# Kernel optimization log

Hardware: AMD Instinct MI355X
Metric: run time of the kernel (lower is better)

Reference implementation:

```python
import jax, jax.numpy as jnp
import numpy as np

V, NLAB, NLAYERS, DI, DM, DS, DD, K = 32000, 9, 2, 768, 1536, 16, 96, 4
B, S = 2, 2048
EPS = 1e-6


def setup_inputs() -> dict:
    key = jax.random.key(0)
    ks = jax.random.split(key, 12)
    n = lambda k, shape, s=0.02: jax.random.normal(k, shape, jnp.float32) * s
    return {
        "input_ids": jax.random.randint(ks[0], (B, S), 0, V, dtype=jnp.int32),
        "attention_mask": jnp.ones((B, S), jnp.int32),
        "emb": n(ks[1], (V, DI)),
        "norm_w": jnp.ones((NLAYERS, DI), jnp.float32),
        "in_proj_w": n(ks[2], (NLAYERS, 2 * DM, DI)),
        "conv_w": n(ks[3], (NLAYERS, DM, K), 0.1),
        "conv_b": jnp.zeros((NLAYERS, DM), jnp.float32),
        "sB_w": n(ks[4], (NLAYERS, DS, DM)),
        "sC_w": n(ks[5], (NLAYERS, DS, DM)),
        "sD1_w": n(ks[6], (NLAYERS, DD, DM)),
        "sD2_w": n(ks[7], (NLAYERS, DM, DD)),
        "A": jnp.tile(jnp.arange(1, DS + 1, dtype=jnp.float32), (NLAYERS, DM, 1)),
        "Dp": jnp.ones((NLAYERS, DM), jnp.float32),
        "out_w": n(ks[8], (NLAYERS, DI, DM)),
        "cls_w": n(ks[9], (NLAB, DI)),
        "cls_b": jnp.zeros((NLAB,), jnp.float32),
    }


def _rmsnorm(x, w):
    return x * jax.lax.rsqrt(jnp.mean(x * x, axis=-1, keepdims=True) + EPS) * w


def _mamba_block(x, norm_w, Wi, cw, cb, WB, WC, W1, W2, A, Dp, Wo):
    # x: (b, l, d_input)
    h = _rmsnorm(x, norm_w)
    a, gate = jnp.split(h @ Wi.T, 2, axis=-1)  # each (b, l, DM)
    # causal depthwise conv1d, kernel K, left-pad K-1 (== Conv1d(pad=K-1)[..., :l])
    L = a.shape[1]
    ap = jnp.pad(a, ((0, 0), (K - 1, 0), (0, 0)))
    conv = cb + sum(ap[:, i:i + L, :] * cw[:, i] for i in range(K))
    a = jax.nn.silu(conv)
    # selective SSM
    Bm = a @ WB.T                                   # (b, l, DS)
    Cm = a @ WC.T                                   # (b, l, DS)
    delta = jax.nn.softplus(Dp + (a @ W1.T) @ W2.T)  # (b, l, DM)
    A_bar = jnp.exp(delta[..., None] * (-A))         # (b, l, DM, DS)
    X_bar = (delta * a)[..., None] * Bm[:, :, None, :]  # (b, l, DM, DS)

    def comb(c1, c2):
        a1, x1 = c1
        a2, x2 = c2
        return a1 * a2, a2 * x1 + x2

    _, hid = jax.lax.associative_scan(comb, (A_bar, X_bar), axis=1)
    y = jnp.einsum('blds,bls->bld', hid, Cm) + Dp * a
    y = y * jax.nn.silu(gate)
    return y @ Wo.T


def _forward(input_ids, attention_mask, emb, norm_w, in_proj_w, conv_w, conv_b,
             sB_w, sC_w, sD1_w, sD2_w, A, Dp, out_w, cls_w, cls_b):
    x = emb[input_ids] * attention_mask[..., None].astype(emb.dtype)
    for i in range(NLAYERS):  # residual Mamba layers
        x = _mamba_block(x, norm_w[i], in_proj_w[i], conv_w[i], conv_b[i],
                         sB_w[i], sC_w[i], sD1_w[i], sD2_w[i], A[i], Dp[i], out_w[i]) + x
    # dropout is identity at inference
    return x @ cls_w.T + cls_b  # logits (b, l, num_labels)


def reference(input_ids, attention_mask, emb, norm_w, in_proj_w, conv_w, conv_b,
              sB_w, sC_w, sD1_w, sD2_w, A, Dp, out_w, cls_w, cls_b):
    return _forward(input_ids, attention_mask, emb, norm_w, in_proj_w, conv_w, conv_b,
                    sB_w, sC_w, sD1_w, sD2_w, A, Dp, out_w, cls_w, cls_b)
```

## Files before the change

### kernel.cpp

```cpp
#include <hip/hip_runtime.h>
#include <hip/hip_bf16.h>
#include <math.h>

#define NLAB 9
#define NL   2
#define DI   768
#define DM   1536
#define DS   16
#define KC   4
#define DD   96
#define BB   2
#define SS   2048
#define TT   (BB*SS)
#define EPSF 1e-6f

#define NCH  64
#define CL   (SS/NCH)

#define NW   128
#define KS   8
#define KSL  (DM/KS)

typedef __attribute__((ext_vector_type(4))) float f32x4;
typedef __attribute__((ext_vector_type(8))) short bf16x8;
typedef __attribute__((ext_vector_type(4))) unsigned short us4;

__device__ __forceinline__ float siluf(float x) { return x / (1.f + __expf(-x)); }
__device__ __forceinline__ float softplusf(float x) { return x > 15.f ? x : log1pf(__expf(x)); }

__device__ __forceinline__ unsigned short f2bf(float f) {
    unsigned u = __float_as_uint(f);
    return (unsigned short)((u + 0x7fffu + ((u >> 16) & 1u)) >> 16);
}

__global__ void f32_to_bf16(const float* __restrict__ src,
                            unsigned short* __restrict__ dst, int n)
{
    int i = (blockIdx.x * 256 + threadIdx.x) * 8;
    if (i >= n) return;
    float4 a = *(const float4*)(src + i);
    float4 b = *(const float4*)(src + i + 4);
    union { unsigned short s[8]; uint4 v; } o;
    o.s[0] = f2bf(a.x); o.s[1] = f2bf(a.y); o.s[2] = f2bf(a.z); o.s[3] = f2bf(a.w);
    o.s[4] = f2bf(b.x); o.s[5] = f2bf(b.y); o.s[6] = f2bf(b.z); o.s[7] = f2bf(b.w);
    *(uint4*)(dst + i) = o.v;
}

__global__ void embed_kernel(const int* __restrict__ ids, const int* __restrict__ mask,
                             const float* __restrict__ emb, float* __restrict__ x)
{
    int t = blockIdx.x;
    int i = threadIdx.x;
    float m = (float)mask[t];
    int id = ids[t];
    float4 v = ((const float4*)(emb + (size_t)id * DI))[i];
    v.x *= m; v.y *= m; v.z *= m; v.w *= m;
    ((float4*)(x + (size_t)t * DI))[i] = v;
}

__global__ void rmsnorm_kernel(const float* __restrict__ x, const float* __restrict__ w,
                               unsigned short* __restrict__ h)
{
    __shared__ float red[4];
    int t = blockIdx.x;
    const float* xr = x + (size_t)t * DI;
    float ss = 0.f;
    for (int i = threadIdx.x; i < DI; i += 256) { float v = xr[i]; ss += v * v; }
    #pragma unroll
    for (int m = 1; m < 64; m <<= 1) ss += __shfl_xor(ss, m, 64);
    if ((threadIdx.x & 63) == 0) red[threadIdx.x >> 6] = ss;
    __syncthreads();
    float scale = rsqrtf((red[0] + red[1] + red[2] + red[3]) * (1.f / DI) + EPSF);
    for (int i = threadIdx.x; i < DI; i += 256)
        h[(size_t)t * DI + i] = f2bf(xr[i] * scale * w[i]);
}

__global__ __launch_bounds__(256) void gemm_bf16(
    const unsigned short* __restrict__ A, const unsigned short* __restrict__ B,
    const float* __restrict__ Rres, const float* __restrict__ bias,
    float* __restrict__ C, int M, int N, int K,
    int lda, int ldb, int ldc, int act, int cstride)
{
    __shared__ unsigned short As[128 * 32];
    __shared__ unsigned short Bs[128 * 32];
    const int tid = threadIdx.x;
    const int wave = tid >> 6, lane = tid & 63;
    const int bm = blockIdx.y * 128, bn = blockIdx.x * 128;
    const int wm = (wave >> 1) * 64, wn = (wave & 1) * 64;
    const int lr = lane & 15, kh = lane >> 4;

    f32x4 acc[4][4] = {};

    const unsigned short* Arow = A + (size_t)bm * lda;
    const unsigned short* Brow = B + (size_t)bn * ldb;

    for (int kt = 0; kt < K; kt += 32) {
        #pragma unroll
        for (int it = 0; it < 2; ++it) {
            int rbase = it * 64 + wave * 16;
            int row = rbase + (lane >> 2);
            int c8 = (lane & 3) * 8;
            __builtin_amdgcn_global_load_lds(
                (const __attribute__((address_space(1))) unsigned int*)(Arow + (size_t)row * lda + kt + c8),
                (__attribute__((address_space(3))) unsigned int*)(As + rbase * 32),
                16, 0, 0);
            __builtin_amdgcn_global_load_lds(
                (const __attribute__((address_space(1))) unsigned int*)(Brow + (size_t)row * ldb + kt + c8),
                (__attribute__((address_space(3))) unsigned int*)(Bs + rbase * 32),
                16, 0, 0);
        }
        __syncthreads();

        bf16x8 af[4], bfr[4];
        #pragma unroll
        for (int i = 0; i < 4; ++i)
            af[i] = *(const bf16x8*)&As[(wm + i * 16 + lr) * 32 + kh * 8];
        #pragma unroll
        for (int j = 0; j < 4; ++j)
            bfr[j] = *(const bf16x8*)&Bs[(wn + j * 16 + lr) * 32 + kh * 8];
        #pragma unroll
        for (int i = 0; i < 4; ++i)
            #pragma unroll
            for (int j = 0; j < 4; ++j)
                acc[i][j] = __builtin_amdgcn_mfma_f32_16x16x32_bf16(af[i], bfr[j], acc[i][j], 0, 0, 0);
        __syncthreads();
    }

    #pragma unroll
    for (int i = 0; i < 4; ++i) {
        #pragma unroll
        for (int j = 0; j < 4; ++j) {
            #pragma unroll
            for (int r = 0; r < 4; ++r) {
                int row = bm + wm + i * 16 + kh * 4 + r;
                int col = bn + wn + j * 16 + lr;
                float v = acc[i][j][r];
                if (bias) v += bias[col];
                if (act == 1) v = softplusf(v);
                if (Rres) v += Rres[(size_t)row * ldc + col];
                C[((size_t)row * ldc + col) * cstride] = v;
            }
        }
    }
}

__global__ __launch_bounds__(256) void gemm_skinny_bf16(
    const unsigned short* __restrict__ A, const unsigned short* __restrict__ B,
    float* __restrict__ Part)
{
    __shared__ unsigned short As[128 * 32];
    __shared__ unsigned short Bs[128 * 32];
    const int tid = threadIdx.x;
    const int wave = tid >> 6, lane = tid & 63;
    const int bm = blockIdx.x * 128;
    const int ks = blockIdx.y;
    const int k0 = ks * KSL;
    const int wm = (wave >> 1) * 64, wn = (wave & 1) * 64;
    const int lr = lane & 15, kh = lane >> 4;

    f32x4 acc[4][4] = {};

    const unsigned short* Arow = A + (size_t)bm * DM;
    const unsigned short* Brow = B;

    for (int kt = 0; kt < KSL; kt += 32) {
        #pragma unroll
        for (int it = 0; it < 2; ++it) {
            int rbase = it * 64 + wave * 16;
            int row = rbase + (lane >> 2);
            int c8 = (lane & 3) * 8;
            __builtin_amdgcn_global_load_lds(
                (const __attribute__((address_space(1))) unsigned int*)(Arow + (size_t)row * DM + k0 + kt + c8),
                (__attribute__((address_space(3))) unsigned int*)(As + rbase * 32),
                16, 0, 0);
            __builtin_amdgcn_global_load_lds(
                (const __attribute__((address_space(1))) unsigned int*)(Brow + (size_t)row * DM + k0 + kt + c8),
                (__attribute__((address_space(3))) unsigned int*)(Bs + rbase * 32),
                16, 0, 0);
        }
        __syncthreads();

        bf16x8 af[4], bfr[4];
        #pragma unroll
        for (int i = 0; i < 4; ++i)
            af[i] = *(const bf16x8*)&As[(wm + i * 16 + lr) * 32 + kh * 8];
        #pragma unroll
        for (int j = 0; j < 4; ++j)
            bfr[j] = *(const bf16x8*)&Bs[(wn + j * 16 + lr) * 32 + kh * 8];
        #pragma unroll
        for (int i = 0; i < 4; ++i)
            #pragma unroll
            for (int j = 0; j < 4; ++j)
                acc[i][j] = __builtin_amdgcn_mfma_f32_16x16x32_bf16(af[i], bfr[j], acc[i][j], 0, 0, 0);
        __syncthreads();
    }

    float* out = Part + (size_t)ks * TT * NW;
    #pragma unroll
    for (int i = 0; i < 4; ++i) {
        #pragma unroll
        for (int j = 0; j < 4; ++j) {
            #pragma unroll
            for (int r = 0; r < 4; ++r) {
                int row = bm + wm + i * 16 + kh * 4 + r;
                int col = wn + j * 16 + lr;
                out[(size_t)row * NW + col] = acc[i][j][r];
            }
        }
    }
}

__global__ void skinny_reduce(const float* __restrict__ Part,
                              float* __restrict__ BCD, unsigned short* __restrict__ dd16)
{
    int idx = blockIdx.x * 256 + threadIdx.x;
    float s = 0.f;
    #pragma unroll
    for (int ks = 0; ks < KS; ++ks)
        s += Part[(size_t)ks * TT * NW + idx];
    BCD[idx] = s;
    int col = idx & (NW - 1);
    if (col >= 32)
        dd16[(size_t)(idx >> 7) * DD + (col - 32)] = f2bf(s);
}

__global__ void conv_silu_kernel(const float* __restrict__ proj, const float* __restrict__ cw,
                                 const float* __restrict__ cb, float2* __restrict__ dav,
                                 unsigned short* __restrict__ aconv16)
{
    int t = blockIdx.x;
    int d = blockIdx.y * 256 + threadIdx.x;
    int p = t & (SS - 1);
    float acc = cb[d];
    #pragma unroll
    for (int j = 0; j < KC; ++j) {
        int pp = p - (KC - 1) + j;
        if (pp >= 0)
            acc += cw[d * KC + j] * proj[(size_t)(t - (KC - 1) + j) * (2 * DM) + d];
    }
    float v = siluf(acc);
    dav[(size_t)t * DM + d].y = v;
    aconv16[(size_t)t * DM + d] = f2bf(v);
}

__global__ void concat_w_kernel(const float* __restrict__ WB, const float* __restrict__ WC,
                                const float* __restrict__ W1, unsigned short* __restrict__ Wcat16)
{
    int l = blockIdx.y;
    int row = blockIdx.x;
    const float* src;
    if (row < 16)      src = WB + (size_t)l * DS * DM + (size_t)row * DM;
    else if (row < 32) src = WC + (size_t)l * DS * DM + (size_t)(row - 16) * DM;
    else               src = W1 + (size_t)l * DD * DM + (size_t)(row - 32) * DM;
    unsigned short* dst = Wcat16 + ((size_t)l * NW + row) * DM;
    for (int i = threadIdx.x; i < DM / 4; i += 256) {
        float4 v = ((const float4*)src)[i];
        us4 u = { f2bf(v.x), f2bf(v.y), f2bf(v.z), f2bf(v.w) };
        *(us4*)(dst + i * 4) = u;
    }
}

__global__ __launch_bounds__(256) void scan_pass1(
    const float2* __restrict__ dav,
    const float* __restrict__ BCD, const float* __restrict__ Amat,
    float2* __restrict__ PQ)
{
    __shared__ float4 sB4[CL][DS / 4];
    int b = blockIdx.z, c = blockIdx.y;
    int d = blockIdx.x * 256 + threadIdx.x;
    size_t rowbase = (size_t)b * SS + (size_t)c * CL;

    for (int i = threadIdx.x; i < CL * DS; i += 256)
        ((float*)sB4)[i] = BCD[(rowbase + (i >> 4)) * NW + (i & 15)];
    __syncthreads();

    float negA[DS], hid[DS];
    #pragma unroll
    for (int s = 0; s < DS; ++s) {
        negA[s] = -Amat[(size_t)d * DS + s];
        hid[s] = 0.f;
    }
    float cum = 0.f;

    const float2* pv = dav + rowbase * DM + d;
    for (int t = 0; t < CL; ++t) {
        float2 da = pv[(size_t)t * DM];
        float dt = da.x, av = da.y;
        cum += dt;
        float xv = dt * av;
        #pragma unroll
        for (int j = 0; j < DS / 4; ++j) {
            float4 bv = sB4[t][j];
            hid[4*j+0] = __expf(dt * negA[4*j+0]) * hid[4*j+0] + xv * bv.x;
            hid[4*j+1] = __expf(dt * negA[4*j+1]) * hid[4*j+1] + xv * bv.y;
            hid[4*j+2] = __expf(dt * negA[4*j+2]) * hid[4*j+2] + xv * bv.z;
            hid[4*j+3] = __expf(dt * negA[4*j+3]) * hid[4*j+3] + xv * bv.w;
        }
    }
    float2* out = PQ + ((size_t)(b * NCH + c) * DM + d) * DS;
    #pragma unroll
    for (int s = 0; s < DS; ++s)
        out[s] = make_float2(__expf(cum * negA[s]), hid[s]);
}

__global__ void scan_carry(float2* __restrict__ PQ)
{
    int idx = blockIdx.x * 256 + threadIdx.x;
    int b = idx / (DM * DS);
    int r = idx - b * (DM * DS);
    float carry = 0.f;
    for (int c = 0; c < NCH; ++c) {
        size_t o = (size_t)(b * NCH + c) * (DM * DS) + r;
        float2 pq = PQ[o];
        PQ[o].x = carry;
        carry = pq.x * carry + pq.y;
    }
}

__global__ __launch_bounds__(256) void scan_pass2(
    const float2* __restrict__ dav,
    const float* __restrict__ BCD,
    const float* __restrict__ proj, const float* __restrict__ Amat,
    const float* __restrict__ Dp, const float2* __restrict__ PQ,
    unsigned short* __restrict__ y)
{
    __shared__ float4 sB4[CL][DS / 4];
    __shared__ float4 sC4[CL][DS / 4];
    int b = blockIdx.z, c = blockIdx.y;
    int d = blockIdx.x * 256 + threadIdx.x;
    size_t rowbase = (size_t)b * SS + (size_t)c * CL;

    for (int i = threadIdx.x; i < CL * DS; i += 256) {
        size_t row = rowbase + (i >> 4);
        ((float*)sB4)[i] = BCD[row * NW + (i & 15)];
        ((float*)sC4)[i] = BCD[row * NW + 16 + (i & 15)];
    }
    __syncthreads();

    float negA[DS], hid[DS];
    const float2* pin = PQ + ((size_t)(b * NCH + c) * DM + d) * DS;
    #pragma unroll
    for (int s = 0; s < DS; ++s) {
        negA[s] = -Amat[(size_t)d * DS + s];
        hid[s] = pin[s].x;
    }
    float Dpd = Dp[d];

    const float2* pv = dav + rowbase * DM + d;
    const float* gp = proj + rowbase * (2 * DM) + DM + d;
    unsigned short* yp = y + rowbase * DM + d;

    for (int t = 0; t < CL; ++t) {
        float2 da = pv[(size_t)t * DM];
        float dt = da.x, av = da.y;
        float g  = gp[(size_t)t * (2 * DM)];
        float xv = dt * av;
        float acc0 = 0.f, acc1 = 0.f, acc2 = 0.f, acc3 = 0.f;
        #pragma unroll
        for (int j = 0; j < DS / 4; ++j) {
            float4 bv = sB4[t][j];
            float4 cv = sC4[t][j];
            hid[4*j+0] = __expf(dt * negA[4*j+0]) * hid[4*j+0] + xv * bv.x;
            hid[4*j+1] = __expf(dt * negA[4*j+1]) * hid[4*j+1] + xv * bv.y;
            hid[4*j+2] = __expf(dt * negA[4*j+2]) * hid[4*j+2] + xv * bv.z;
            hid[4*j+3] = __expf(dt * negA[4*j+3]) * hid[4*j+3] + xv * bv.w;
            acc0 += hid[4*j+0] * cv.x;
            acc1 += hid[4*j+1] * cv.y;
            acc2 += hid[4*j+2] * cv.z;
            acc3 += hid[4*j+3] * cv.w;
        }
        float contrib = (acc0 + acc1) + (acc2 + acc3);
        yp[(size_t)t * DM] = f2bf((contrib + Dpd * av) * siluf(g));
    }
}

__global__ void cls_kernel(const float* __restrict__ x, const float* __restrict__ W,
                           const float* __restrict__ bias, float* __restrict__ out)
{
    int t = blockIdx.x;
    int lane = threadIdx.x;
    const float* xr = x + (size_t)t * DI;
    float acc[NLAB];
    #pragma unroll
    for (int n = 0; n < NLAB; ++n) acc[n] = 0.f;
    for (int i = lane; i < DI; i += 64) {
        float xv = xr[i];
        #pragma unroll
        for (int n = 0; n < NLAB; ++n) acc[n] += xv * W[(size_t)n * DI + i];
    }
    #pragma unroll
    for (int n = 0; n < NLAB; ++n)
        #pragma unroll
        for (int m = 1; m < 64; m <<= 1) acc[n] += __shfl_xor(acc[n], m, 64);
    if (lane < NLAB) out[(size_t)t * NLAB + lane] = acc[lane] + bias[lane];
}

extern "C" void kernel_launch(void* const* d_in, const int* in_sizes, int n_in,
                              void* d_out, int out_size, void* d_ws, size_t ws_size,
                              hipStream_t stream)
{
    const int*   ids    = (const int*)d_in[0];
    const int*   mask   = (const int*)d_in[1];
    const float* emb    = (const float*)d_in[2];
    const float* norm_w = (const float*)d_in[3];
    const float* Wi     = (const float*)d_in[4];
    const float* conv_w = (const float*)d_in[5];
    const float* conv_b = (const float*)d_in[6];
    const float* sB_w   = (const float*)d_in[7];
    const float* sC_w   = (const float*)d_in[8];
    const float* sD1_w  = (const float*)d_in[9];
    const float* sD2_w  = (const float*)d_in[10];
    const float* Amat   = (const float*)d_in[11];
    const float* Dp     = (const float*)d_in[12];
    const float* out_w  = (const float*)d_in[13];
    const float* cls_w  = (const float*)d_in[14];
    const float* cls_b  = (const float*)d_in[15];
    float* logits = (float*)d_out;

    float* ws = (float*)d_ws;
    size_t off = 0;
    float* x     = ws + off; off += (size_t)TT * DI;
    float* proj  = ws + off; off += (size_t)TT * 2 * DM;
    float2* dav  = (float2*)(ws + off); off += (size_t)TT * DM * 2;
    float* BCD   = ws + off; off += (size_t)TT * NW;
    size_t scratch_sz = (size_t)BB * NCH * DM * DS * 2;
    size_t part_sz = (size_t)KS * TT * NW;
    if (part_sz > scratch_sz) scratch_sz = part_sz;
    float* Part  = ws + off;
    float2* PQ   = (float2*)(ws + off); off += scratch_sz;
    unsigned short* y16     = (unsigned short*)(ws + off); off += (size_t)TT * DM / 2;
    unsigned short* aconv16 = (unsigned short*)(ws + off); off += (size_t)TT * DM / 2;
    unsigned short* Wi16    = (unsigned short*)(ws + off); off += (size_t)NL * 2 * DM * DI / 2;
    unsigned short* Wo16    = (unsigned short*)(ws + off); off += (size_t)NL * DI * DM / 2;
    unsigned short* W216    = (unsigned short*)(ws + off); off += (size_t)NL * DM * DD / 2;
    unsigned short* dd16    = (unsigned short*)(ws + off); off += (size_t)TT * DD / 2;
    unsigned short* Wcat16  = (unsigned short*)(ws + off); off += (size_t)NL * NW * DM / 2;
    if (ws_size < off * sizeof(float)) return;

    unsigned short* h16 = (unsigned short*)dav;

    embed_kernel<<<TT, DI / 4, 0, stream>>>(ids, mask, emb, x);
    concat_w_kernel<<<dim3(NW, NL), 256, 0, stream>>>(sB_w, sC_w, sD1_w, Wcat16);

    f32_to_bf16<<<(NL * 2 * DM * DI / 8 + 255) / 256, 256, 0, stream>>>(Wi, Wi16, NL * 2 * DM * DI);
    f32_to_bf16<<<(NL * DI * DM / 8 + 255) / 256, 256, 0, stream>>>(out_w, Wo16, NL * DI * DM);
    f32_to_bf16<<<(NL * DM * DD / 8 + 255) / 256, 256, 0, stream>>>(sD2_w, W216, NL * DM * DD);

    for (int l = 0; l < NL; ++l) {
        const float* cw_l  = conv_w + (size_t)l * DM * KC;
        const float* cb_l  = conv_b + (size_t)l * DM;
        const float* A_l   = Amat  + (size_t)l * DM * DS;
        const float* Dp_l  = Dp    + (size_t)l * DM;
        const float* nw_l  = norm_w + (size_t)l * DI;
        const unsigned short* Wi16_l  = Wi16  + (size_t)l * 2 * DM * DI;
        const unsigned short* Wo16_l  = Wo16  + (size_t)l * DI * DM;
        const unsigned short* W216_l  = W216  + (size_t)l * DM * DD;
        const unsigned short* Wcat16_l = Wcat16 + (size_t)l * NW * DM;

        rmsnorm_kernel<<<TT, 256, 0, stream>>>(x, nw_l, h16);

        gemm_bf16<<<dim3(2 * DM / 128, TT / 128), 256, 0, stream>>>(
            h16, Wi16_l, nullptr, nullptr, proj, TT, 2 * DM, DI, DI, DI, 2 * DM, 0, 1);

        conv_silu_kernel<<<dim3(TT, DM / 256), 256, 0, stream>>>(proj, cw_l, cb_l, dav, aconv16);

        gemm_skinny_bf16<<<dim3(TT / 128, KS), 256, 0, stream>>>(aconv16, Wcat16_l, Part);
        skinny_reduce<<<TT * NW / 256, 256, 0, stream>>>(Part, BCD, dd16);

        gemm_bf16<<<dim3(DM / 128, TT / 128), 256, 0, stream>>>(
            dd16, W216_l, nullptr, Dp_l, (float*)dav, TT, DM, DD, DD, DD, DM, 1, 2);

        scan_pass1<<<dim3(DM / 256, NCH, BB), 256, 0, stream>>>(dav, BCD, A_l, PQ);
        scan_carry<<<BB * DM * DS / 256, 256, 0, stream>>>(PQ);
        scan_pass2<<<dim3(DM / 256, NCH, BB), 256, 0, stream>>>(
            dav, BCD, proj, A_l, Dp_l, PQ, y16);

        gemm_bf16<<<dim3(DI / 128, TT / 128), 256, 0, stream>>>(
            y16, Wo16_l, x, nullptr, x, TT, DI, DM, DM, DM, DI, 0, 1);
    }

    cls_kernel<<<TT, 64, 0, stream>>>(x, cls_w, cls_b, logits);
}
```

Measured before the change: 786.2 us.

## Double-buffer LDS tiles in GEMMs and split interleaved delta/activation buffer

```diff
diff --git a/kernel.cpp b/kernel.cpp
--- a/kernel.cpp
+++ b/kernel.cpp
@@ -75,14 +75,45 @@
         h[(size_t)t * DI + i] = f2bf(xr[i] * scale * w[i]);
 }
 
+#define STAGE_TILE(AS, BS, KT) do {                                                           \
+    _Pragma("unroll")                                                                         \
+    for (int it = 0; it < 2; ++it) {                                                          \
+        int rbase = it * 64 + wave * 16;                                                      \
+        int row = rbase + (lane >> 2);                                                        \
+        int c8 = (lane & 3) * 8;                                                              \
+        __builtin_amdgcn_global_load_lds(                                                     \
+            (const __attribute__((address_space(1))) unsigned int*)(Arow + (size_t)row * lda + (KT) + c8), \
+            (__attribute__((address_space(3))) unsigned int*)((AS) + rbase * 32), 16, 0, 0);  \
+        __builtin_amdgcn_global_load_lds(                                                     \
+            (const __attribute__((address_space(1))) unsigned int*)(Brow + (size_t)row * ldb + (KT) + c8), \
+            (__attribute__((address_space(3))) unsigned int*)((BS) + rbase * 32), 16, 0, 0);  \
+    } } while (0)
+
+#define COMPUTE_TILE(AS, BS) do {                                                             \
+    bf16x8 af[4], bfr[4];                                                                     \
+    _Pragma("unroll")                                                                         \
+    for (int i = 0; i < 4; ++i)                                                               \
+        af[i] = *(const bf16x8*)&(AS)[(wm + i * 16 + lr) * 32 + kh * 8];                      \
+    _Pragma("unroll")                                                                         \
+    for (int j = 0; j < 4; ++j)                                                               \
+        bfr[j] = *(const bf16x8*)&(BS)[(wn + j * 16 + lr) * 32 + kh * 8];                     \
+    _Pragma("unroll")                                                                         \
+    for (int i = 0; i < 4; ++i)                                                               \
+        _Pragma("unroll")                                                                     \
+        for (int j = 0; j < 4; ++j)                                                           \
+            acc[i][j] = __builtin_amdgcn_mfma_f32_16x16x32_bf16(af[i], bfr[j], acc[i][j], 0, 0, 0); \
+    } while (0)
+
 __global__ __launch_bounds__(256) void gemm_bf16(
     const unsigned short* __restrict__ A, const unsigned short* __restrict__ B,
     const float* __restrict__ Rres, const float* __restrict__ bias,
     float* __restrict__ C, int M, int N, int K,
     int lda, int ldb, int ldc, int act, int cstride)
 {
-    __shared__ unsigned short As[128 * 32];
-    __shared__ unsigned short Bs[128 * 32];
+    __shared__ unsigned short As0[128 * 32];
+    __shared__ unsigned short Bs0[128 * 32];
+    __shared__ unsigned short As1[128 * 32];
+    __shared__ unsigned short Bs1[128 * 32];
     const int tid = threadIdx.x;
     const int wave = tid >> 6, lane = tid & 63;
     const int bm = blockIdx.y * 128, bn = blockIdx.x * 128;
@@ -94,36 +125,21 @@
     const unsigned short* Arow = A + (size_t)bm * lda;
     const unsigned short* Brow = B + (size_t)bn * ldb;
 
-    for (int kt = 0; kt < K; kt += 32) {
-        #pragma unroll
-        for (int it = 0; it < 2; ++it) {
-            int rbase = it * 64 + wave * 16;
-            int row = rbase + (lane >> 2);
-            int c8 = (lane & 3) * 8;
-            __builtin_amdgcn_global_load_lds(
-                (const __attribute__((address_space(1))) unsigned int*)(Arow + (size_t)row * lda + kt + c8),
-                (__attribute__((address_space(3))) unsigned int*)(As + rbase * 32),
-                16, 0, 0);
-            __builtin_amdgcn_global_load_lds(
-                (const __attribute__((address_space(1))) unsigned int*)(Brow + (size_t)row * ldb + kt + c8),
-                (__attribute__((address_space(3))) unsigned int*)(Bs + rbase * 32),
-                16, 0, 0);
-        }
+    STAGE_TILE(As0, Bs0, 0);
+    __syncthreads();
+
+    int kt = 0;
+    while (true) {
+        if (kt + 32 < K) STAGE_TILE(As1, Bs1, kt + 32);
+        COMPUTE_TILE(As0, Bs0);
         __syncthreads();
-
-        bf16x8 af[4], bfr[4];
-        #pragma unroll
-        for (int i = 0; i < 4; ++i)
-            af[i] = *(const bf16x8*)&As[(wm + i * 16 + lr) * 32 + kh * 8];
-        #pragma unroll
-        for (int j = 0; j < 4; ++j)
-            bfr[j] = *(const bf16x8*)&Bs[(wn + j * 16 + lr) * 32 + kh * 8];
-        #pragma unroll
-        for (int i = 0; i < 4; ++i)
-            #pragma unroll
-            for (int j = 0; j < 4; ++j)
-                acc[i][j] = __builtin_amdgcn_mfma_f32_16x16x32_bf16(af[i], bfr[j], acc[i][j], 0, 0, 0);
+        kt += 32;
+        if (kt >= K) break;
+        if (kt + 32 < K) STAGE_TILE(As0, Bs0, kt + 32);
+        COMPUTE_TILE(As1, Bs1);
         __syncthreads();
+        kt += 32;
+        if (kt >= K) break;
     }
 
     #pragma unroll
@@ -148,8 +164,10 @@
     const unsigned short* __restrict__ A, const unsigned short* __restrict__ B,
     float* __restrict__ Part)
 {
-    __shared__ unsigned short As[128 * 32];
-    __shared__ unsigned short Bs[128 * 32];
+    __shared__ unsigned short As0[128 * 32];
+    __shared__ unsigned short Bs0[128 * 32];
+    __shared__ unsigned short As1[128 * 32];
+    __shared__ unsigned short Bs1[128 * 32];
     const int tid = threadIdx.x;
     const int wave = tid >> 6, lane = tid & 63;
     const int bm = blockIdx.x * 128;
@@ -157,42 +175,28 @@
     const int k0 = ks * KSL;
     const int wm = (wave >> 1) * 64, wn = (wave & 1) * 64;
     const int lr = lane & 15, kh = lane >> 4;
+    const int lda = DM, ldb = DM;
 
     f32x4 acc[4][4] = {};
 
     const unsigned short* Arow = A + (size_t)bm * DM;
     const unsigned short* Brow = B;
 
-    for (int kt = 0; kt < KSL; kt += 32) {
-        #pragma unroll
-        for (int it = 0; it < 2; ++it) {
-            int rbase = it * 64 + wave * 16;
-            int row = rbase + (lane >> 2);
-            int c8 = (lane & 3) * 8;
-            __builtin_amdgcn_global_load_lds(
-                (const __attribute__((address_space(1))) unsigned int*)(Arow + (size_t)row * DM + k0 + kt + c8),
-                (__attribute__((address_space(3))) unsigned int*)(As + rbase * 32),
-                16, 0, 0);
-            __builtin_amdgcn_global_load_lds(
-                (const __attribute__((address_space(1))) unsigned int*)(Brow + (size_t)row * DM + k0 + kt + c8),
-                (__attribute__((address_space(3))) unsigned int*)(Bs + rbase * 32),
-                16, 0, 0);
-        }
+    STAGE_TILE(As0, Bs0, k0);
+    __syncthreads();
+
+    int kt = 0;
+    while (true) {
+        if (kt + 32 < KSL) STAGE_TILE(As1, Bs1, k0 + kt + 32);
+        COMPUTE_TILE(As0, Bs0);
         __syncthreads();
-
-        bf16x8 af[4], bfr[4];
-        #pragma unroll
-        for (int i = 0; i < 4; ++i)
-            af[i] = *(const bf16x8*)&As[(wm + i * 16 + lr) * 32 + kh * 8];
-        #pragma unroll
-        for (int j = 0; j < 4; ++j)
-            bfr[j] = *(const bf16x8*)&Bs[(wn + j * 16 + lr) * 32 + kh * 8];
-        #pragma unroll
-        for (int i = 0; i < 4; ++i)
-            #pragma unroll
-            for (int j = 0; j < 4; ++j)
-                acc[i][j] = __builtin_amdgcn_mfma_f32_16x16x32_bf16(af[i], bfr[j], acc[i][j], 0, 0, 0);
+        kt += 32;
+        if (kt >= KSL) break;
+        if (kt + 32 < KSL) STAGE_TILE(As0, Bs0, k0 + kt + 32);
+        COMPUTE_TILE(As1, Bs1);
         __syncthreads();
+        kt += 32;
+        if (kt >= KSL) break;
     }
 
     float* out = Part + (size_t)ks * TT * NW;
@@ -225,7 +229,7 @@
 }
 
 __global__ void conv_silu_kernel(const float* __restrict__ proj, const float* __restrict__ cw,
-                                 const float* __restrict__ cb, float2* __restrict__ dav,
+                                 const float* __restrict__ cb, float* __restrict__ av,
                                  unsigned short* __restrict__ aconv16)
 {
     int t = blockIdx.x;
@@ -239,7 +243,7 @@
             acc += cw[d * KC + j] * proj[(size_t)(t - (KC - 1) + j) * (2 * DM) + d];
     }
     float v = siluf(acc);
-    dav[(size_t)t * DM + d].y = v;
+    av[(size_t)t * DM + d] = v;
     aconv16[(size_t)t * DM + d] = f2bf(v);
 }
 
@@ -261,7 +265,7 @@
 }
 
 __global__ __launch_bounds__(256) void scan_pass1(
-    const float2* __restrict__ dav,
+    const float* __restrict__ dtv, const float* __restrict__ av,
     const float* __restrict__ BCD, const float* __restrict__ Amat,
     float2* __restrict__ PQ)
 {
@@ -282,12 +286,13 @@
     }
     float cum = 0.f;
 
-    const float2* pv = dav + rowbase * DM + d;
+    const float* pd = dtv + rowbase * DM + d;
+    const float* pa = av  + rowbase * DM + d;
     for (int t = 0; t < CL; ++t) {
-        float2 da = pv[(size_t)t * DM];
-        float dt = da.x, av = da.y;
+        float dt = pd[(size_t)t * DM];
+        float avv = pa[(size_t)t * DM];
         cum += dt;
-        float xv = dt * av;
+        float xv = dt * avv;
         #pragma unroll
         for (int j = 0; j < DS / 4; ++j) {
             float4 bv = sB4[t][j];
@@ -318,7 +323,7 @@
 }
 
 __global__ __launch_bounds__(256) void scan_pass2(
-    const float2* __restrict__ dav,
+    const float* __restrict__ dtv, const float* __restrict__ av,
     const float* __restrict__ BCD,
     const float* __restrict__ proj, const float* __restrict__ Amat,
     const float* __restrict__ Dp, const float2* __restrict__ PQ,
@@ -346,15 +351,16 @@
     }
     float Dpd = Dp[d];
 
-    const float2* pv = dav + rowbase * DM + d;
+    const float* pd = dtv + rowbase * DM + d;
+    const float* pa = av  + rowbase * DM + d;
     const float* gp = proj + rowbase * (2 * DM) + DM + d;
     unsigned short* yp = y + rowbase * DM + d;
 
     for (int t = 0; t < CL; ++t) {
-        float2 da = pv[(size_t)t * DM];
-        float dt = da.x, av = da.y;
+        float dt = pd[(size_t)t * DM];
+        float avv = pa[(size_t)t * DM];
         float g  = gp[(size_t)t * (2 * DM)];
-        float xv = dt * av;
+        float xv = dt * avv;
         float acc0 = 0.f, acc1 = 0.f, acc2 = 0.f, acc3 = 0.f;
         #pragma unroll
         for (int j = 0; j < DS / 4; ++j) {
@@ -370,7 +376,7 @@
             acc3 += hid[4*j+3] * cv.w;
         }
         float contrib = (acc0 + acc1) + (acc2 + acc3);
-        yp[(size_t)t * DM] = f2bf((contrib + Dpd * av) * siluf(g));
+        yp[(size_t)t * DM] = f2bf((contrib + Dpd * avv) * siluf(g));
     }
 }
 
@@ -421,7 +427,8 @@
     size_t off = 0;
     float* x     = ws + off; off += (size_t)TT * DI;
     float* proj  = ws + off; off += (size_t)TT * 2 * DM;
-    float2* dav  = (float2*)(ws + off); off += (size_t)TT * DM * 2;
+    float* dtv   = ws + off; off += (size_t)TT * DM;
+    float* av    = ws + off; off += (size_t)TT * DM;
     float* BCD   = ws + off; off += (size_t)TT * NW;
     size_t scratch_sz = (size_t)BB * NCH * DM * DS * 2;
     size_t part_sz = (size_t)KS * TT * NW;
@@ -437,7 +444,7 @@
     unsigned short* Wcat16  = (unsigned short*)(ws + off); off += (size_t)NL * NW * DM / 2;
     if (ws_size < off * sizeof(float)) return;
 
-    unsigned short* h16 = (unsigned short*)dav;
+    unsigned short* h16 = (unsigned short*)dtv;
 
     embed_kernel<<<TT, DI / 4, 0, stream>>>(ids, mask, emb, x);
     concat_w_kernel<<<dim3(NW, NL), 256, 0, stream>>>(sB_w, sC_w, sD1_w, Wcat16);
@@ -462,18 +469,18 @@
         gemm_bf16<<<dim3(2 * DM / 128, TT / 128), 256, 0, stream>>>(
             h16, Wi16_l, nullptr, nullptr, proj, TT, 2 * DM, DI, DI, DI, 2 * DM, 0, 1);
 
-        conv_silu_kernel<<<dim3(TT, DM / 256), 256, 0, stream>>>(proj, cw_l, cb_l, dav, aconv16);
+        conv_silu_kernel<<<dim3(TT, DM / 256), 256, 0, stream>>>(proj, cw_l, cb_l, av, aconv16);
 
         gemm_skinny_bf16<<<dim3(TT / 128, KS), 256, 0, stream>>>(aconv16, Wcat16_l, Part);
         skinny_reduce<<<TT * NW / 256, 256, 0, stream>>>(Part, BCD, dd16);
 
         gemm_bf16<<<dim3(DM / 128, TT / 128), 256, 0, stream>>>(
-            dd16, W216_l, nullptr, Dp_l, (float*)dav, TT, DM, DD, DD, DD, DM, 1, 2);
-
-        scan_pass1<<<dim3(DM / 256, NCH, BB), 256, 0, stream>>>(dav, BCD, A_l, PQ);
+            dd16, W216_l, nullptr, Dp_l, dtv, TT, DM, DD, DD, DD, DM, 1, 1);
+
+        scan_pass1<<<dim3(DM / 256, NCH, BB), 256, 0, stream>>>(dtv, av, BCD, A_l, PQ);
         scan_carry<<<BB * DM * DS / 256, 256, 0, stream>>>(PQ);
         scan_pass2<<<dim3(DM / 256, NCH, BB), 256, 0, stream>>>(
-            dav, BCD, proj, A_l, Dp_l, PQ, y16);
+            dtv, av, BCD, proj, A_l, Dp_l, PQ, y16);
 
         gemm_bf16<<<dim3(DI / 128, TT / 128), 256, 0, stream>>>(
             y16, Wo16_l, x, nullptr, x, TT, DI, DM, DM, DM, DI, 0, 1);
```

Measured after the change: 753.7 us. 4.1% less time.
